# Kernel optimization log

Measured on AMD Instinct MI355X. Metric: run time of the kernel, lower is better.

The kernel has to match this reference:

```python
import jax, jax.numpy as jnp
import numpy as np

E = 8          # n_experts
K = 2          # n_activated_experts (top_k)
CAP_FACTOR = 1.25


def _expert_mlp(x, cond, mask, W1, W2):
    # x: [t, d], cond: [t, dc], mask: [t] -> [t, d]
    h = jax.nn.gelu(jnp.concatenate([x, cond], axis=-1) @ W1)
    return (h @ W2) * mask[:, None]


def setup_inputs() -> dict:
    key = jax.random.key(0)
    ks = jax.random.split(key, 8)
    b, n, d, dc, dff = 4, 2048, 1024, 256, 4096
    return {
        "x": jax.random.normal(ks[0], (b, n, d), jnp.float32),
        "cond": jax.random.normal(ks[1], (b, n, dc), jnp.float32),
        "mask": jnp.ones((b, n), jnp.float32),
        "Wr": jax.random.normal(ks[2], (d, E), jnp.float32) * 0.02,
        "W1s": jax.random.normal(ks[3], (d + dc, dff), jnp.float32) * 0.02,
        "W2s": jax.random.normal(ks[4], (dff, d), jnp.float32) * 0.02,
        "W1e": jax.random.normal(ks[5], (E, d + dc, dff), jnp.float32) * 0.02,
        "W2e": jax.random.normal(ks[6], (E, dff, d), jnp.float32) * 0.02,
    }


def reference(x, cond, mask, Wr, W1s, W2s, W1e, W2e):
    b, n, d = x.shape
    T = b * n
    cap = int(CAP_FACTOR * K * T / E)  # expert_capacity (static)

    xf = x.reshape(T, d)
    cf = cond.reshape(T, -1)
    mf = mask.reshape(T)

    # ---- router: softmax then top-k, normalized weights ----
    scores = jax.nn.softmax(xf @ Wr, axis=-1)              # [T, E]
    w, idx = jax.lax.top_k(scores, K)                      # [T, K]
    w = w / jnp.sum(w, axis=-1, keepdims=True)

    # ---- shared expert ----
    x_shared = _expert_mlp(xf, cf, mf, W1s, W2s)           # [T, d]

    # ---- indices_and_bins: stable sort by expert id + histogram/cumsum ----
    te = idx.reshape(-1)                                   # [T*K]
    order = jnp.argsort(te)                                # stable sort
    bin_ids = te[order]                                    # [T*K]
    tpe = jnp.zeros((E,), jnp.int32).at[te].add(1)         # tokens_per_expert
    starts = jnp.cumsum(tpe) - tpe                         # exclusive cumsum
    pos = jnp.arange(T * K) - starts[bin_ids]              # slot within expert bin
    tok = order // K                                       # source token row
    valid = pos < cap                                      # capacity drop

    # ---- binned_gather into [E, cap, *] buffers (drops overflow tokens) ----
    xg = jnp.zeros((E, cap, d), xf.dtype).at[bin_ids, pos].set(xf[tok], mode="drop")
    cg = jnp.zeros((E, cap, cf.shape[-1]), cf.dtype).at[bin_ids, pos].set(cf[tok], mode="drop")
    mg = jnp.zeros((E, cap), mf.dtype).at[bin_ids, pos].set(mf[tok], mode="drop")

    # ---- per-expert dense compute (grouped GEMM via einsum) ----
    inp = jnp.concatenate([xg, cg], axis=-1)               # [E, cap, d+dc]
    h = jax.nn.gelu(jnp.einsum("eci,eih->ech", inp, W1e))  # [E, cap, dff]
    y = jnp.einsum("ech,ehd->ecd", h, W2e) * mg[..., None] # [E, cap, d]

    # ---- binned_scatter combine with expert weights ----
    vals = y[bin_ids, jnp.minimum(pos, cap - 1)]           # [T*K, d]
    vals = vals * (w.reshape(-1)[order] * valid)[:, None]
    x_moe = jnp.zeros((T, d), xf.dtype).at[tok].add(vals)

    out = (x_shared + x_moe * K) / (K + 1)                 # normalize_expert_weights=True
    return out.reshape(b, n, d)
```

## Files before the change

### kernel.cpp

```cpp
#include <hip/hip_runtime.h>


typedef unsigned short u16;
typedef unsigned int u32;
typedef __bf16 bf16x8 __attribute__((ext_vector_type(8)));
typedef float f32x4 __attribute__((ext_vector_type(4)));

constexpr int T_TOK = 8192;
constexpr int DIM   = 1024;
constexpr int DCOND = 256;
constexpr int DFF   = 4096;
constexpr int NEXP  = 8;
constexpr int CAP   = 2560;

__device__ __forceinline__ float b2f(u16 u) {
    union { u32 u; float f; } v; v.u = (u32)u << 16; return v.f;
}
__device__ __forceinline__ u16 f2b(float f) {
    union { float f; u32 u; } v; v.f = f;
    u32 r = (v.u + 0x7fffu + ((v.u >> 16) & 1u)) >> 16;
    return (u16)r;
}
__device__ __forceinline__ float gelu_f(float x) {
    if (!(x == x)) x = 0.f;
    x = fminf(1e4f, fmaxf(-1e4f, x));
    float z = 0.7978845608028654f * (x + 0.044715f * x * x * x);
    float e = __expf(2.0f * z);
    float th = 1.0f - 2.0f / (e + 1.0f);
    return 0.5f * x * (1.0f + th);
}

__device__ __forceinline__ void gload16(const u16* g, u16* l) {
    __builtin_amdgcn_global_load_lds(
        (const __attribute__((address_space(1))) void*)g,
        (__attribute__((address_space(3))) void*)l, 16, 0, 0);
}

template <int IMM>
__device__ __forceinline__ bf16x8 dsr(u32 addr) {
    bf16x8 d;
    asm volatile("ds_read_b128 %0, %1 offset:%2" : "=v"(d) : "v"(addr), "n"(IMM));
    return d;
}
template <int N>
__device__ __forceinline__ void vmwait() {
    asm volatile("s_waitcnt vmcnt(%0)" :: "n"(N) : "memory");
}
__device__ __forceinline__ void lgkm0() {
    asm volatile("s_waitcnt lgkmcnt(0)" ::: "memory");
}

__global__ void moe_probe(const u16* __restrict__ x, int* __restrict__ flag) {
    const int lane = threadIdx.x;
    int cnt = 0;
    for (int i = lane; i < 4096; i += 64) {
        int e = (x[i] >> 7) & 0xFF;
        cnt += (e >= 0xC8);
    }
#pragma unroll
    for (int off = 32; off; off >>= 1) cnt += __shfl_xor(cnt, off, 64);
    if (lane == 0) flag[0] = (cnt > 8) ? 1 : 0;
}

__global__ __launch_bounds__(256) void moe_cvt(
    const void* __restrict__ in, u16* __restrict__ out,
    const int* __restrict__ flag)
{
    const long long i = ((long long)blockIdx.x * 256 + threadIdx.x) * 8;
    if (flag[0]) {
        const float* s = (const float*)in + i;
        float4 a = *(const float4*)s;
        float4 b = *(const float4*)(s + 4);
        __align__(16) u16 t8[8];
        t8[0] = f2b(a.x); t8[1] = f2b(a.y); t8[2] = f2b(a.z); t8[3] = f2b(a.w);
        t8[4] = f2b(b.x); t8[5] = f2b(b.y); t8[6] = f2b(b.z); t8[7] = f2b(b.w);
        *(uint4*)(out + i) = *(const uint4*)t8;
    } else {
        *(uint4*)(out + i) = *(const uint4*)((const u16*)in + i);
    }
}

__global__ __launch_bounds__(256) void moe_router(
    const void* __restrict__ xv, const void* __restrict__ Wrv,
    const int* __restrict__ flag,
    float* __restrict__ wbuf, int* __restrict__ idxbuf)
{
    const int t = blockIdx.x * 4 + (threadIdx.x >> 6);
    const int lane = threadIdx.x & 63;
    const bool isf32 = flag[0] != 0;

    float acc[NEXP];
#pragma unroll
    for (int e = 0; e < NEXP; ++e) acc[e] = 0.f;

    if (isf32) {
        const float* xr = (const float*)xv + (long long)t * DIM;
        const float* Wr = (const float*)Wrv;
        for (int it = 0; it < DIM / 64; ++it) {
            int d = it * 64 + lane;
            float xvv = xr[d];
            float4 wa = *(const float4*)(Wr + d * NEXP);
            float4 wb = *(const float4*)(Wr + d * NEXP + 4);
            acc[0] += xvv * wa.x; acc[1] += xvv * wa.y;
            acc[2] += xvv * wa.z; acc[3] += xvv * wa.w;
            acc[4] += xvv * wb.x; acc[5] += xvv * wb.y;
            acc[6] += xvv * wb.z; acc[7] += xvv * wb.w;
        }
    } else {
        const u16* xr = (const u16*)xv + (long long)t * DIM;
        const u16* Wr = (const u16*)Wrv;
        for (int it = 0; it < DIM / 64; ++it) {
            int d = it * 64 + lane;
            float xvv = b2f(xr[d]);
            uint4 wvv = *(const uint4*)(Wr + d * NEXP);
            const u16* ws = (const u16*)&wvv;
#pragma unroll
            for (int e = 0; e < NEXP; ++e) acc[e] += xvv * b2f(ws[e]);
        }
    }
#pragma unroll
    for (int off = 32; off; off >>= 1)
#pragma unroll
        for (int e = 0; e < NEXP; ++e) acc[e] += __shfl_xor(acc[e], off, 64);

    if (lane == 0) {
        float b1 = -3.4e38f, b2 = -3.4e38f; int i1 = 0, i2 = 0;
#pragma unroll
        for (int e = 0; e < NEXP; ++e) {
            float v = acc[e];
            if (v > b1) { b2 = b1; i2 = i1; b1 = v; i1 = e; }
            else if (v > b2) { b2 = v; i2 = e; }
        }
        float p2 = expf(b2 - b1);
        float inv = 1.0f / (1.0f + p2);
        wbuf[2 * t] = inv;       wbuf[2 * t + 1] = p2 * inv;
        idxbuf[2 * t] = i1;      idxbuf[2 * t + 1] = i2;
    }
}

__global__ void moe_bins(const int* __restrict__ idxbuf, int* __restrict__ slot_of,
                         int* __restrict__ token_of, int* __restrict__ rows_e)
{
    const int lane = threadIdx.x;
    const unsigned long long lmask = (1ull << lane) - 1ull;
    int cnt[NEXP];
#pragma unroll
    for (int q = 0; q < NEXP; ++q) cnt[q] = 0;

    for (int base = 0; base < T_TOK * 2; base += 256) {
        int e4[4];
#pragma unroll
        for (int u = 0; u < 4; ++u) e4[u] = idxbuf[base + u * 64 + lane];
#pragma unroll
        for (int u = 0; u < 4; ++u) {
            int e = e4[u];
            int ent = base + u * 64 + lane;
            int my = 0;
#pragma unroll
            for (int q = 0; q < NEXP; ++q) {
                unsigned long long bal = __ballot(e == q);
                if (e == q) my = cnt[q] + (int)__popcll(bal & lmask);
                cnt[q] += (int)__popcll(bal);
            }
            slot_of[ent] = my;
            if (my < CAP) token_of[e * CAP + my] = ent >> 1;
        }
    }
    if (lane == 0) {
#pragma unroll
        for (int q = 0; q < NEXP; ++q) rows_e[q] = cnt[q] < CAP ? cnt[q] : CAP;
    }
}

__global__ __launch_bounds__(256) void moe_transpose(
    const void* __restrict__ inv, u16* __restrict__ out, const int* __restrict__ flag,
    int R, int C, int zBase, long long inBatch, long long outBatch)
{
    const int zi = zBase + blockIdx.z;
    const bool isf32 = flag[0] != 0;
    out += (long long)blockIdx.z * outBatch;
    const int c0 = blockIdx.x * 64, r0 = blockIdx.y * 64;

    __shared__ __align__(16) u16 tile[64][66];

    for (int g = threadIdx.x; g < 512; g += 256) {
        int r = g >> 3, c8 = (g & 7) * 8;
        long long off = (long long)zi * inBatch + (long long)(r0 + r) * C + c0 + c8;
        if (isf32) {
            const float* s = (const float*)inv + off;
            float4 a = *(const float4*)s;
            float4 b = *(const float4*)(s + 4);
            tile[r][c8 + 0] = f2b(a.x); tile[r][c8 + 1] = f2b(a.y);
            tile[r][c8 + 2] = f2b(a.z); tile[r][c8 + 3] = f2b(a.w);
            tile[r][c8 + 4] = f2b(b.x); tile[r][c8 + 5] = f2b(b.y);
            tile[r][c8 + 6] = f2b(b.z); tile[r][c8 + 7] = f2b(b.w);
        } else {
            uint4 v = *(const uint4*)((const u16*)inv + off);
            const u16* s = (const u16*)&v;
#pragma unroll
            for (int j = 0; j < 8; ++j) tile[r][c8 + j] = s[j];
        }
    }
    __syncthreads();
    for (int g = threadIdx.x; g < 512; g += 256) {
        int oc = g >> 3, orr = (g & 7) * 8;
        __align__(16) u16 vals[8];
#pragma unroll
        for (int j = 0; j < 8; ++j) vals[j] = tile[orr + j][oc];
        *(uint4*)&out[(long long)(c0 + oc) * R + r0 + orr] = *(const uint4*)vals;
    }
}


#define AIMM(buf, qm, f8) ((buf) * 32768 + (qm) * 16384 + (f8) * 2048)

#define READ_A(buf, qm) do { \
    a[0][0] = dsr<AIMM(buf, qm, 0)>(aA0); a[0][1] = dsr<AIMM(buf, qm, 0)>(aA1); \
    a[1][0] = dsr<AIMM(buf, qm, 1)>(aA0); a[1][1] = dsr<AIMM(buf, qm, 1)>(aA1); \
    a[2][0] = dsr<AIMM(buf, qm, 2)>(aA0); a[2][1] = dsr<AIMM(buf, qm, 2)>(aA1); \
    a[3][0] = dsr<AIMM(buf, qm, 3)>(aA0); a[3][1] = dsr<AIMM(buf, qm, 3)>(aA1); \
} while (0)

#define READ_B(buf, qn) do { \
    if constexpr (BN == 256) { \
        b[qn][0][0] = dsr<(buf) * 32768 + (qn) * 16384 + 0>(aB0); \
        b[qn][0][1] = dsr<(buf) * 32768 + (qn) * 16384 + 0>(aB1); \
        b[qn][1][0] = dsr<(buf) * 32768 + (qn) * 16384 + 2048>(aB0); \
        b[qn][1][1] = dsr<(buf) * 32768 + (qn) * 16384 + 2048>(aB1); \
    } else { \
        b[qn][0][0] = dsr<(buf) * 16384 + (qn) * 8192>(aB0); \
        b[qn][0][1] = dsr<(buf) * 16384 + (qn) * 8192>(aB1); \
    } \
} while (0)

#define MFMA_Q(qm, qn) do { \
    _Pragma("unroll") for (int f9 = 0; f9 < 4; ++f9) \
    _Pragma("unroll") for (int n9 = 0; n9 < N9; ++n9) \
    _Pragma("unroll") for (int k9 = 0; k9 < 2; ++k9) \
        acc[(qm) * 4 + f9][(qn) * N9 + n9] = __builtin_amdgcn_mfma_f32_16x16x32_bf16( \
            a[f9][k9], b[qn][n9][k9], acc[(qm) * 4 + f9][(qn) * N9 + n9], 0, 0, 0); \
} while (0)

#define STAGE_A(buf, qm, kt) do { \
    const int ke7 = (kt) * 64; \
    _Pragma("unroll") for (int i7 = 0; i7 < 2; ++i7) { \
        const u16* src7; \
        if constexpr (MODE >= 1) { \
            src7 = (ke7 < DIM) \
                ? (const u16*)(A1b + offA1[i7][qm] + ke7 * 2) \
                : (const u16*)(A2b + offA2[i7][qm] + (ke7 - DIM) * 2); \
        } else { \
            src7 = (const u16*)(A1b + offA1[i7][qm] + ke7 * 2); \
        } \
        gload16(src7, &As[buf][qm][(wave * 64 + i7 * 512) * 8]); \
    } \
} while (0)

#define STAGE_B(buf, qn, kt) do { \
    const int ke7 = (kt) * 64; \
    _Pragma("unroll") for (int i7 = 0; i7 < SB; ++i7) \
        gload16((const u16*)(BTb + offB[i7][qn] + ke7 * 2), \
                &Bs[buf][qn][(wave * 64 + i7 * 512) * 8]); \
} while (0)

#define PH_OPEN() __builtin_amdgcn_sched_barrier(0)
#define PH_MID() do { \
    __builtin_amdgcn_sched_barrier(0); \
    __builtin_amdgcn_s_barrier(); \
    lgkm0(); \
    __builtin_amdgcn_sched_barrier(0); \
    __builtin_amdgcn_s_setprio(1); \
} while (0)
#define PH_CLOSE() do { \
    __builtin_amdgcn_s_setprio(0); \
    __builtin_amdgcn_sched_barrier(0); \
    __builtin_amdgcn_s_barrier(); \
} while (0)
#define PH_CLOSE_VM() do { \
    __builtin_amdgcn_s_setprio(0); \
    vmwait<VMN>(); \
    __builtin_amdgcn_sched_barrier(0); \
    __builtin_amdgcn_s_barrier(); \
} while (0)

template <int MODE, int KTOT, int BN>
__global__ __launch_bounds__(512, 2) void moe_gemm_8p(
    const u16* __restrict__ A1, const u16* __restrict__ A2,
    const u16* __restrict__ BT, u16* __restrict__ C,
    const int* __restrict__ tok_base, const int* __restrict__ rows_base,
    int ldC, long long aBatch, long long bBatch, long long cBatch)
{
    constexpr int NKT = KTOT / 64;
    static_assert((NKT & 1) == 0 && NKT >= 4, "K tiling");
    constexpr int N9  = BN / 128;
    constexpr int SB  = BN / 128;
    constexpr int VMN = 2 + 2 * SB;

    const u32 nwg  = gridDim.x * gridDim.y;
    const u32 flat = blockIdx.y * gridDim.x + blockIdx.x;
    const u32 swz  = (flat & 7u) * (nwg >> 3) + (flat >> 3);
    const int bx = (int)(swz % gridDim.x);
    const int by = (int)(swz / gridDim.x);

    const int z = blockIdx.z;
    int rows = 1 << 30;
    if (rows_base) {
        rows = rows_base[z];
        if (by * 256 >= rows) return;
    }

    __shared__ __align__(16) u16 As[2][2][8192];
    __shared__ __align__(16) u16 Bs[2][2][BN * 32];

    const int tid  = threadIdx.x;
    const int lane = tid & 63;
    const int wave = tid >> 6;
    const int wmw  = wave >> 2;
    const int wnw  = wave & 3;
    const int m0 = by * 256;
    const int n0 = bx * BN;

    const char* A1b = (const char*)(MODE == 0 ? A1 + (long long)z * aBatch : A1);
    const char* A2b = (const char*)A2;
    const char* BTb = (const char*)(BT + (long long)z * bBatch);

    u32 offA1[2][2], offA2[2][2], offB[SB][2];
#pragma unroll
    for (int i = 0; i < 2; ++i) {
        const int g = tid + i * 512;
        const int wm = g >> 9, r = (g >> 3) & 63, c16 = g & 7;
        const int cs = (c16 ^ (r & 7)) * 8;
#pragma unroll
        for (int qm = 0; qm < 2; ++qm) {
            const int rg = m0 + wm * 128 + qm * 64 + r;
            if constexpr (MODE == 2) {
                const int* tok = tok_base + (long long)z * CAP;
                const int tk = (rg < rows) ? tok[rg] : 0;
                offA1[i][qm] = (u32)((tk * DIM + cs) * 2);
                offA2[i][qm] = (u32)((tk * DCOND + cs) * 2);
            } else if constexpr (MODE == 1) {
                offA1[i][qm] = (u32)((rg * DIM + cs) * 2);
                offA2[i][qm] = (u32)((rg * DCOND + cs) * 2);
            } else {
                offA1[i][qm] = (u32)(((long long)rg * KTOT + cs) * 2);
                offA2[i][qm] = 0;
            }
        }
    }
#pragma unroll
    for (int i = 0; i < SB; ++i) {
        const int g = tid + i * 512;
        int wn, c;
        if constexpr (BN == 256) { wn = g >> 8; c = (g >> 3) & 31; }
        else                     { wn = g >> 7; c = (g >> 3) & 15; }
        const int c16 = g & 7;
        const int cs = (c16 ^ (c & 7)) * 8;
#pragma unroll
        for (int qn = 0; qn < 2; ++qn) {
            const int cbl = (BN == 256) ? (wn * 64 + qn * 32 + c)
                                        : (wn * 32 + qn * 16 + c);
            offB[i][qn] = (u32)(((long long)(n0 + cbl) * KTOT + cs) * 2);
        }
    }

    const u32 AsB = (u32)(size_t)(__attribute__((address_space(3))) u16*)&As[0][0][0];
    const u32 BsB = (u32)(size_t)(__attribute__((address_space(3))) u16*)&Bs[0][0][0];
    const int lrow = lane & 15;
    const int x0 = (((lane >> 4) + 0) ^ (lane & 7)) << 4;
    const int x4 = (((lane >> 4) + 4) ^ (lane & 7)) << 4;
    const u32 aA0 = AsB + (u32)((wmw * 64 + lrow) * 128 + x0);
    const u32 aA1 = AsB + (u32)((wmw * 64 + lrow) * 128 + x4);
    const int bro = (BN == 256 ? wnw * 32 : wnw * 16) + lrow;
    const u32 aB0 = BsB + (u32)(bro * 128 + x0);
    const u32 aB1 = BsB + (u32)(bro * 128 + x4);

    f32x4 acc[8][2 * N9];
#pragma unroll
    for (int m = 0; m < 8; ++m)
#pragma unroll
        for (int n = 0; n < 2 * N9; ++n) { f32x4 zv = {0.f, 0.f, 0.f, 0.f}; acc[m][n] = zv; }

    bf16x8 a[4][2];
    bf16x8 b[2][N9][2];

    STAGE_A(0, 0, 0); STAGE_B(0, 0, 0); STAGE_A(0, 1, 0); STAGE_B(0, 1, 0);
    STAGE_A(1, 0, 1); STAGE_B(1, 0, 1); STAGE_B(1, 1, 1);
    vmwait<VMN>();
    __builtin_amdgcn_sched_barrier(0);
    __builtin_amdgcn_s_barrier();

#pragma unroll 1
    for (int t = 0; t < NKT / 2; ++t) {
        const int k2 = 2 * t;
        const int kA = (k2 + 2 < NKT) ? k2 + 2 : NKT - 1;
        const int kB = (k2 + 3 < NKT) ? k2 + 3 : NKT - 1;
        PH_OPEN(); READ_A(0, 0); READ_B(0, 0); STAGE_A(1, 1, k2 + 1);
        PH_MID();  MFMA_Q(0, 0); PH_CLOSE();
        PH_OPEN(); READ_B(0, 1); STAGE_A(0, 0, kA);
        PH_MID();  MFMA_Q(0, 1); PH_CLOSE();
        PH_OPEN(); READ_A(0, 1); STAGE_B(0, 0, kA);
        PH_MID();  MFMA_Q(1, 0); PH_CLOSE();
        PH_OPEN(); STAGE_B(0, 1, kA);
        PH_MID();  MFMA_Q(1, 1); PH_CLOSE_VM();
        PH_OPEN(); READ_A(1, 0); READ_B(1, 0); STAGE_A(0, 1, kA);
        PH_MID();  MFMA_Q(0, 0); PH_CLOSE();
        PH_OPEN(); READ_B(1, 1); STAGE_A(1, 0, kB);
        PH_MID();  MFMA_Q(0, 1); PH_CLOSE();
        PH_OPEN(); READ_A(1, 1); STAGE_B(1, 0, kB);
        PH_MID();  MFMA_Q(1, 0); PH_CLOSE();
        PH_OPEN(); STAGE_B(1, 1, kB);
        PH_MID();  MFMA_Q(1, 1); PH_CLOSE_VM();
    }

    u16* Cz = C + (long long)z * cBatch;
#pragma unroll
    for (int m = 0; m < 8; ++m) {
        const int rowb = m0 + wmw * 128 + (m >> 2) * 64 + (m & 3) * 16 + (lane >> 4) * 4;
#pragma unroll
        for (int n = 0; n < 2 * N9; ++n) {
            int col;
            if constexpr (BN == 256)
                col = n0 + wnw * 64 + (n >> 1) * 32 + (n & 1) * 16 + (lane & 15);
            else
                col = n0 + wnw * 32 + n * 16 + (lane & 15);
#pragma unroll
            for (int rr = 0; rr < 4; ++rr) {
                float v = acc[m][n][rr];
                if constexpr (MODE >= 1) v = gelu_f(v);
                Cz[(long long)(rowb + rr) * ldC + col] = f2b(v);
            }
        }
    }
}

__global__ __launch_bounds__(256) void moe_combine(
    const u16* __restrict__ xs, const u16* __restrict__ y,
    const float* __restrict__ wbuf, const int* __restrict__ idxbuf,
    const int* __restrict__ slot_of, const void* __restrict__ maskv,
    void* __restrict__ outv, const int* __restrict__ flag)
{
    const int t = blockIdx.x;
    const int c = threadIdx.x * 4;
    const bool isf32 = flag[0] != 0;
    const float mk = isf32 ? ((const float*)maskv)[t] : b2f(((const u16*)maskv)[t]);

    int e1 = idxbuf[2 * t], e2 = idxbuf[2 * t + 1];
    int s1 = slot_of[2 * t], s2 = slot_of[2 * t + 1];
    float w1 = wbuf[2 * t], w2 = wbuf[2 * t + 1];
    float g1 = (s1 < CAP) ? w1 : 0.f;
    float g2 = (s2 < CAP) ? w2 : 0.f;
    int r1 = s1 < CAP ? s1 : CAP - 1;
    int r2 = s2 < CAP ? s2 : CAP - 1;

    uint2 xvv = *(const uint2*)(xs + (long long)t * DIM + c);
    uint2 y1 = *(const uint2*)(y + ((long long)e1 * CAP + r1) * DIM + c);
    uint2 y2 = *(const uint2*)(y + ((long long)e2 * CAP + r2) * DIM + c);
    const u16* xp = (const u16*)&xvv;
    const u16* p1 = (const u16*)&y1;
    const u16* p2 = (const u16*)&y2;

    float o[4];
#pragma unroll
    for (int q = 0; q < 4; ++q) {
        float v = (b2f(xp[q]) + 2.f * (g1 * b2f(p1[q]) + g2 * b2f(p2[q]))) * mk * (1.f / 3.f);
        o[q] = (v == v) ? v : 0.f;
    }
    if (isf32) {
        float4 o4 = {o[0], o[1], o[2], o[3]};
        *(float4*)((float*)outv + (long long)t * DIM + c) = o4;
    } else {
        __align__(8) u16 ov[4];
#pragma unroll
        for (int q = 0; q < 4; ++q) ov[q] = f2b(o[q]);
        *(uint2*)((u16*)outv + (long long)t * DIM + c) = *(const uint2*)ov;
    }
}

extern "C" void kernel_launch(void* const* d_in, const int* in_sizes, int n_in,
                              void* d_out, int out_size, void* d_ws, size_t ws_size,
                              hipStream_t stream)
{
    const void* x    = d_in[0];
    const void* cond = d_in[1];
    const void* mask = d_in[2];
    const void* Wr   = d_in[3];
    const void* W1s  = d_in[4];
    const void* W2s  = d_in[5];
    const void* W1e  = d_in[6];
    const void* W2e  = d_in[7];

    const int KIN = DIM + DCOND;
    const int EGX = 3;

    char* p = (char*)d_ws;
    u16* W1sT   = (u16*)p; p += (long long)DFF * KIN * 2;
    u16* W2sT   = (u16*)p; p += (long long)DIM * DFF * 2;
    u16* W1eT   = (u16*)p; p += (long long)EGX * DFF * KIN * 2;
    u16* W2eT   = (u16*)p; p += (long long)EGX * DIM * DFF * 2;
    u16* h      = (u16*)p; p += (long long)T_TOK * DFF * 2;
    u16* xs     = (u16*)p; p += (long long)T_TOK * DIM * 2;
    u16* y      = (u16*)p; p += (long long)NEXP * CAP * DIM * 2;
    u16* xb     = (u16*)p; p += (long long)T_TOK * DIM * 2;
    u16* cb     = (u16*)p; p += (long long)T_TOK * DCOND * 2;
    float* wbuf = (float*)p; p += T_TOK * 2 * sizeof(float);
    int* idxbuf = (int*)p;   p += T_TOK * 2 * sizeof(int);
    int* slot_of = (int*)p;  p += T_TOK * 2 * sizeof(int);
    int* token_of = (int*)p; p += NEXP * CAP * sizeof(int);
    int* rows_e = (int*)p;   p += 256;
    int* flag   = (int*)p;   p += 256;
    (void)ws_size; (void)in_sizes; (void)n_in; (void)out_size;

    dim3 b256(256);
    dim3 b512(512);

    moe_probe<<<dim3(1), dim3(64), 0, stream>>>((const u16*)x, flag);

    moe_cvt<<<dim3(T_TOK * DIM / (256 * 8)), b256, 0, stream>>>(x, xb, flag);
    moe_cvt<<<dim3(T_TOK * DCOND / (256 * 8)), b256, 0, stream>>>(cond, cb, flag);

    moe_router<<<dim3(T_TOK / 4), b256, 0, stream>>>(x, Wr, flag, wbuf, idxbuf);
    moe_bins<<<dim3(1), dim3(64), 0, stream>>>(idxbuf, slot_of, token_of, rows_e);

    moe_transpose<<<dim3(DFF / 64, KIN / 64, 1), b256, 0, stream>>>(
        W1s, W1sT, flag, KIN, DFF, 0, 0, 0);
    moe_transpose<<<dim3(DIM / 64, DFF / 64, 1), b256, 0, stream>>>(
        W2s, W2sT, flag, DFF, DIM, 0, 0, 0);

    moe_gemm_8p<1, 1280, 256><<<dim3(DFF / 256, T_TOK / 256, 1), b512, 0, stream>>>(
        xb, cb, W1sT, h, nullptr, nullptr, DFF, 0, 0, 0);
    moe_gemm_8p<0, 4096, 128><<<dim3(DIM / 128, T_TOK / 256, 1), b512, 0, stream>>>(
        h, nullptr, W2sT, xs, nullptr, nullptr, DIM, 0, 0, 0);

    const int gsz[3] = {3, 3, 2};
    int gb = 0;
    for (int gi = 0; gi < 3; ++gi) {
        const int eg = gsz[gi];
        moe_transpose<<<dim3(DFF / 64, KIN / 64, eg), b256, 0, stream>>>(
            W1e, W1eT, flag, KIN, DFF, gb,
            (long long)KIN * DFF, (long long)DFF * KIN);
        moe_transpose<<<dim3(DIM / 64, DFF / 64, eg), b256, 0, stream>>>(
            W2e, W2eT, flag, DFF, DIM, gb,
            (long long)DFF * DIM, (long long)DIM * DFF);

        moe_gemm_8p<2, 1280, 256><<<dim3(DFF / 256, CAP / 256, eg), b512, 0, stream>>>(
            xb, cb, W1eT, h, token_of + (long long)gb * CAP, rows_e + gb,
            DFF, 0, (long long)DFF * KIN, (long long)CAP * DFF);
        moe_gemm_8p<0, 4096, 128><<<dim3(DIM / 128, CAP / 256, eg), b512, 0, stream>>>(
            h, nullptr, W2eT, y + (long long)gb * CAP * DIM, nullptr, rows_e + gb,
            DIM, (long long)CAP * DFF, (long long)DIM * DFF, (long long)CAP * DIM);
        gb += eg;
    }

    moe_combine<<<dim3(T_TOK), b256, 0, stream>>>(xs, y, wbuf, idxbuf, slot_of, mask, d_out, flag);
}
```

Baseline: 1.154 ms.

## Double-buffer A fragments and overlap LDS reads with MFMA phases in GEMM loop

Restructures the 8-phase main loop of the grouped GEMM so LDS fragment reads for the next quadrant are issued before the barrier of the current MFMA phase. Partial lgkmcnt waits replace the full lgkmcnt(0) drain, letting reads stay in flight. The A register fragments are now double-buffered per M-quadrant, the prologue prefetches the first fragments, and the MFMA loop order puts k outermost. This is meant to hide LDS latency behind matrix math, at the cost of more VGPRs (risking spills at 2 waves/SIMD) and a subtle wait-count schedule that could be wrong.

After: 1.307 ms. 13.3% more time.

```diff
diff --git a/kernel.cpp b/kernel.cpp
--- a/kernel.cpp
+++ b/kernel.cpp
@@ -46,8 +46,9 @@
 __device__ __forceinline__ void vmwait() {
     asm volatile("s_waitcnt vmcnt(%0)" :: "n"(N) : "memory");
 }
-__device__ __forceinline__ void lgkm0() {
-    asm volatile("s_waitcnt lgkmcnt(0)" ::: "memory");
+template <int N>
+__device__ __forceinline__ void lgkmw() {
+    asm volatile("s_waitcnt lgkmcnt(%0)" :: "n"(N) : "memory");
 }
 
 __global__ void moe_probe(const u16* __restrict__ x, int* __restrict__ flag) {
@@ -215,10 +216,10 @@
 #define AIMM(buf, qm, f8) ((buf) * 32768 + (qm) * 16384 + (f8) * 2048)
 
 #define READ_A(buf, qm) do { \
-    a[0][0] = dsr<AIMM(buf, qm, 0)>(aA0); a[0][1] = dsr<AIMM(buf, qm, 0)>(aA1); \
-    a[1][0] = dsr<AIMM(buf, qm, 1)>(aA0); a[1][1] = dsr<AIMM(buf, qm, 1)>(aA1); \
-    a[2][0] = dsr<AIMM(buf, qm, 2)>(aA0); a[2][1] = dsr<AIMM(buf, qm, 2)>(aA1); \
-    a[3][0] = dsr<AIMM(buf, qm, 3)>(aA0); a[3][1] = dsr<AIMM(buf, qm, 3)>(aA1); \
+    a[qm][0][0] = dsr<AIMM(buf, qm, 0)>(aA0); a[qm][0][1] = dsr<AIMM(buf, qm, 0)>(aA1); \
+    a[qm][1][0] = dsr<AIMM(buf, qm, 1)>(aA0); a[qm][1][1] = dsr<AIMM(buf, qm, 1)>(aA1); \
+    a[qm][2][0] = dsr<AIMM(buf, qm, 2)>(aA0); a[qm][2][1] = dsr<AIMM(buf, qm, 2)>(aA1); \
+    a[qm][3][0] = dsr<AIMM(buf, qm, 3)>(aA0); a[qm][3][1] = dsr<AIMM(buf, qm, 3)>(aA1); \
 } while (0)
 
 #define READ_B(buf, qn) do { \
@@ -234,11 +235,11 @@
 } while (0)
 
 #define MFMA_Q(qm, qn) do { \
+    _Pragma("unroll") for (int k9 = 0; k9 < 2; ++k9) \
     _Pragma("unroll") for (int f9 = 0; f9 < 4; ++f9) \
     _Pragma("unroll") for (int n9 = 0; n9 < N9; ++n9) \
-    _Pragma("unroll") for (int k9 = 0; k9 < 2; ++k9) \
         acc[(qm) * 4 + f9][(qn) * N9 + n9] = __builtin_amdgcn_mfma_f32_16x16x32_bf16( \
-            a[f9][k9], b[qn][n9][k9], acc[(qm) * 4 + f9][(qn) * N9 + n9], 0, 0, 0); \
+            a[qm][f9][k9], b[qn][n9][k9], acc[(qm) * 4 + f9][(qn) * N9 + n9], 0, 0, 0); \
 } while (0)
 
 #define STAGE_A(buf, qm, kt) do { \
@@ -263,24 +264,30 @@
                 &Bs[buf][qn][(wave * 64 + i7 * 512) * 8]); \
 } while (0)
 
-#define PH_OPEN() __builtin_amdgcn_sched_barrier(0)
-#define PH_MID() do { \
+#define PH_MID(n) do { \
     __builtin_amdgcn_sched_barrier(0); \
     __builtin_amdgcn_s_barrier(); \
-    lgkm0(); \
-    __builtin_amdgcn_sched_barrier(0); \
+    lgkmw<n>(); \
+    __builtin_amdgcn_sched_barrier(0); \
+    __builtin_amdgcn_s_setprio(1); \
+} while (0)
+#define PH_MIDN() do { \
+    __builtin_amdgcn_sched_barrier(0); \
+    __builtin_amdgcn_s_barrier(); \
     __builtin_amdgcn_s_setprio(1); \
 } while (0)
 #define PH_CLOSE() do { \
     __builtin_amdgcn_s_setprio(0); \
     __builtin_amdgcn_sched_barrier(0); \
     __builtin_amdgcn_s_barrier(); \
+    __builtin_amdgcn_sched_barrier(0); \
 } while (0)
 #define PH_CLOSE_VM() do { \
     __builtin_amdgcn_s_setprio(0); \
-    vmwait<VMN>(); \
+    vmwait<VMW>(); \
     __builtin_amdgcn_sched_barrier(0); \
     __builtin_amdgcn_s_barrier(); \
+    __builtin_amdgcn_sched_barrier(0); \
 } while (0)
 
 template <int MODE, int KTOT, int BN>
@@ -294,7 +301,8 @@
     static_assert((NKT & 1) == 0 && NKT >= 4, "K tiling");
     constexpr int N9  = BN / 128;
     constexpr int SB  = BN / 128;
-    constexpr int VMN = 2 + 2 * SB;
+    constexpr int VMW = 2 + SB;
+    constexpr int RB  = 2 * SB;
 
     const u32 nwg  = gridDim.x * gridDim.y;
     const u32 flat = blockIdx.y * gridDim.x + blockIdx.x;
@@ -380,37 +388,41 @@
 #pragma unroll
         for (int n = 0; n < 2 * N9; ++n) { f32x4 zv = {0.f, 0.f, 0.f, 0.f}; acc[m][n] = zv; }
 
-    bf16x8 a[4][2];
+    bf16x8 a[2][4][2];
     bf16x8 b[2][N9][2];
 
     STAGE_A(0, 0, 0); STAGE_B(0, 0, 0); STAGE_A(0, 1, 0); STAGE_B(0, 1, 0);
-    STAGE_A(1, 0, 1); STAGE_B(1, 0, 1); STAGE_B(1, 1, 1);
-    vmwait<VMN>();
+    STAGE_A(1, 0, 1); STAGE_B(1, 0, 1); STAGE_A(1, 1, 1); STAGE_B(1, 1, 1);
+    vmwait<4 + 2 * SB>();
     __builtin_amdgcn_sched_barrier(0);
     __builtin_amdgcn_s_barrier();
+    __builtin_amdgcn_sched_barrier(0);
+    READ_A(0, 0); READ_B(0, 0);
 
 #pragma unroll 1
     for (int t = 0; t < NKT / 2; ++t) {
         const int k2 = 2 * t;
         const int kA = (k2 + 2 < NKT) ? k2 + 2 : NKT - 1;
         const int kB = (k2 + 3 < NKT) ? k2 + 3 : NKT - 1;
-        PH_OPEN(); READ_A(0, 0); READ_B(0, 0); STAGE_A(1, 1, k2 + 1);
-        PH_MID();  MFMA_Q(0, 0); PH_CLOSE();
-        PH_OPEN(); READ_B(0, 1); STAGE_A(0, 0, kA);
-        PH_MID();  MFMA_Q(0, 1); PH_CLOSE();
-        PH_OPEN(); READ_A(0, 1); STAGE_B(0, 0, kA);
-        PH_MID();  MFMA_Q(1, 0); PH_CLOSE();
-        PH_OPEN(); STAGE_B(0, 1, kA);
-        PH_MID();  MFMA_Q(1, 1); PH_CLOSE_VM();
-        PH_OPEN(); READ_A(1, 0); READ_B(1, 0); STAGE_A(0, 1, kA);
-        PH_MID();  MFMA_Q(0, 0); PH_CLOSE();
-        PH_OPEN(); READ_B(1, 1); STAGE_A(1, 0, kB);
-        PH_MID();  MFMA_Q(0, 1); PH_CLOSE();
-        PH_OPEN(); READ_A(1, 1); STAGE_B(1, 0, kB);
-        PH_MID();  MFMA_Q(1, 0); PH_CLOSE();
-        PH_OPEN(); STAGE_B(1, 1, kB);
-        PH_MID();  MFMA_Q(1, 1); PH_CLOSE_VM();
-    }
+        READ_B(0, 1);
+        PH_MID(RB);  MFMA_Q(0, 0); PH_CLOSE();
+        READ_A(0, 1); STAGE_A(0, 0, kA);
+        PH_MID(8);   MFMA_Q(0, 1); PH_CLOSE();
+        STAGE_B(0, 0, kA);
+        PH_MID(0);   MFMA_Q(1, 0); PH_CLOSE_VM();
+        READ_A(1, 0); READ_B(1, 0); STAGE_B(0, 1, kA); STAGE_A(0, 1, kA);
+        PH_MIDN();   MFMA_Q(1, 1); PH_CLOSE();
+        READ_B(1, 1);
+        PH_MID(RB);  MFMA_Q(0, 0); PH_CLOSE();
+        READ_A(1, 1); STAGE_A(1, 0, kB);
+        PH_MID(8);   MFMA_Q(0, 1); PH_CLOSE();
+        STAGE_B(1, 0, kB);
+        PH_MID(0);   MFMA_Q(1, 0); PH_CLOSE_VM();
+        READ_A(0, 0); READ_B(0, 0); STAGE_B(1, 1, kB); STAGE_A(1, 1, kB);
+        PH_MIDN();   MFMA_Q(1, 1); PH_CLOSE();
+    }
+    lgkmw<0>();
+    vmwait<0>();
 
     u16* Cz = C + (long long)z * cBatch;
 #pragma unroll
```

## Restructure GEMM main loop from eight phases to four per K pair

Applied to the files above, without the earlier changes.

The GEMM inner loop is regrouped from eight barrier-delimited phases per two K tiles into four. Each phase now loads both B quadrants and issues MFMAs over a full M half, so fewer s_barriers and sched_barriers are needed. A final vmwait is added after the loop. The aim is lower synchronization overhead and longer MFMA bursts, at the cost of more registers live for B fragments and coarser interleaving of global loads with compute.

Result: no change. 1.142 ms (-1.0%).

```diff
diff --git a/kernel.cpp b/kernel.cpp
--- a/kernel.cpp
+++ b/kernel.cpp
@@ -233,12 +233,13 @@
     } \
 } while (0)
 
-#define MFMA_Q(qm, qn) do { \
+#define MFMA_P(qm) do { \
+    _Pragma("unroll") for (int k9 = 0; k9 < 2; ++k9) \
     _Pragma("unroll") for (int f9 = 0; f9 < 4; ++f9) \
+    _Pragma("unroll") for (int q9 = 0; q9 < 2; ++q9) \
     _Pragma("unroll") for (int n9 = 0; n9 < N9; ++n9) \
-    _Pragma("unroll") for (int k9 = 0; k9 < 2; ++k9) \
-        acc[(qm) * 4 + f9][(qn) * N9 + n9] = __builtin_amdgcn_mfma_f32_16x16x32_bf16( \
-            a[f9][k9], b[qn][n9][k9], acc[(qm) * 4 + f9][(qn) * N9 + n9], 0, 0, 0); \
+        acc[(qm) * 4 + f9][q9 * N9 + n9] = __builtin_amdgcn_mfma_f32_16x16x32_bf16( \
+            a[f9][k9], b[q9][n9][k9], acc[(qm) * 4 + f9][q9 * N9 + n9], 0, 0, 0); \
 } while (0)
 
 #define STAGE_A(buf, qm, kt) do { \
@@ -263,28 +264,23 @@
                 &Bs[buf][qn][(wave * 64 + i7 * 512) * 8]); \
 } while (0)
 
-#define PH_OPEN() __builtin_amdgcn_sched_barrier(0)
-#define PH_MID() do { \
-    __builtin_amdgcn_sched_barrier(0); \
-    __builtin_amdgcn_s_barrier(); \
+#define PH_WAIT() do { \
     lgkm0(); \
     __builtin_amdgcn_sched_barrier(0); \
     __builtin_amdgcn_s_setprio(1); \
 } while (0)
-#define PH_CLOSE() do { \
+#define PH_END() do { \
     __builtin_amdgcn_s_setprio(0); \
-    __builtin_amdgcn_sched_barrier(0); \
     __builtin_amdgcn_s_barrier(); \
 } while (0)
-#define PH_CLOSE_VM() do { \
+#define PH_END_VM() do { \
     __builtin_amdgcn_s_setprio(0); \
-    vmwait<VMN>(); \
-    __builtin_amdgcn_sched_barrier(0); \
+    vmwait<VMW>(); \
     __builtin_amdgcn_s_barrier(); \
 } while (0)
 
 template <int MODE, int KTOT, int BN>
-__global__ __launch_bounds__(512, 2) void moe_gemm_8p(
+__global__ __launch_bounds__(512, 2) void moe_gemm_4p(
     const u16* __restrict__ A1, const u16* __restrict__ A2,
     const u16* __restrict__ BT, u16* __restrict__ C,
     const int* __restrict__ tok_base, const int* __restrict__ rows_base,
@@ -294,7 +290,7 @@
     static_assert((NKT & 1) == 0 && NKT >= 4, "K tiling");
     constexpr int N9  = BN / 128;
     constexpr int SB  = BN / 128;
-    constexpr int VMN = 2 + 2 * SB;
+    constexpr int VMW = 2 + 2 * SB;
 
     const u32 nwg  = gridDim.x * gridDim.y;
     const u32 flat = blockIdx.y * gridDim.x + blockIdx.x;
@@ -385,8 +381,7 @@
 
     STAGE_A(0, 0, 0); STAGE_B(0, 0, 0); STAGE_A(0, 1, 0); STAGE_B(0, 1, 0);
     STAGE_A(1, 0, 1); STAGE_B(1, 0, 1); STAGE_B(1, 1, 1);
-    vmwait<VMN>();
-    __builtin_amdgcn_sched_barrier(0);
+    vmwait<VMW>();
     __builtin_amdgcn_s_barrier();
 
 #pragma unroll 1
@@ -394,23 +389,20 @@
         const int k2 = 2 * t;
         const int kA = (k2 + 2 < NKT) ? k2 + 2 : NKT - 1;
         const int kB = (k2 + 3 < NKT) ? k2 + 3 : NKT - 1;
-        PH_OPEN(); READ_A(0, 0); READ_B(0, 0); STAGE_A(1, 1, k2 + 1);
-        PH_MID();  MFMA_Q(0, 0); PH_CLOSE();
-        PH_OPEN(); READ_B(0, 1); STAGE_A(0, 0, kA);
-        PH_MID();  MFMA_Q(0, 1); PH_CLOSE();
-        PH_OPEN(); READ_A(0, 1); STAGE_B(0, 0, kA);
-        PH_MID();  MFMA_Q(1, 0); PH_CLOSE();
-        PH_OPEN(); STAGE_B(0, 1, kA);
-        PH_MID();  MFMA_Q(1, 1); PH_CLOSE_VM();
-        PH_OPEN(); READ_A(1, 0); READ_B(1, 0); STAGE_A(0, 1, kA);
-        PH_MID();  MFMA_Q(0, 0); PH_CLOSE();
-        PH_OPEN(); READ_B(1, 1); STAGE_A(1, 0, kB);
-        PH_MID();  MFMA_Q(0, 1); PH_CLOSE();
-        PH_OPEN(); READ_A(1, 1); STAGE_B(1, 0, kB);
-        PH_MID();  MFMA_Q(1, 0); PH_CLOSE();
-        PH_OPEN(); STAGE_B(1, 1, kB);
-        PH_MID();  MFMA_Q(1, 1); PH_CLOSE_VM();
-    }
+        STAGE_A(1, 1, k2 + 1);
+        READ_A(0, 0); READ_B(0, 0); READ_B(0, 1);
+        PH_WAIT(); MFMA_P(0); PH_END();
+        STAGE_A(0, 0, kA); STAGE_B(0, 0, kA); STAGE_B(0, 1, kA);
+        READ_A(0, 1);
+        PH_WAIT(); MFMA_P(1); PH_END_VM();
+        STAGE_A(0, 1, kA);
+        READ_A(1, 0); READ_B(1, 0); READ_B(1, 1);
+        PH_WAIT(); MFMA_P(0); PH_END();
+        STAGE_A(1, 0, kB); STAGE_B(1, 0, kB); STAGE_B(1, 1, kB);
+        READ_A(1, 1);
+        PH_WAIT(); MFMA_P(1); PH_END_VM();
+    }
+    vmwait<0>();
 
     u16* Cz = C + (long long)z * cBatch;
 #pragma unroll
@@ -526,9 +518,9 @@
     moe_transpose<<<dim3(DIM / 64, DFF / 64, 1), b256, 0, stream>>>(
         W2s, W2sT, flag, DFF, DIM, 0, 0, 0);
 
-    moe_gemm_8p<1, 1280, 256><<<dim3(DFF / 256, T_TOK / 256, 1), b512, 0, stream>>>(
+    moe_gemm_4p<1, 1280, 256><<<dim3(DFF / 256, T_TOK / 256, 1), b512, 0, stream>>>(
         xb, cb, W1sT, h, nullptr, nullptr, DFF, 0, 0, 0);
-    moe_gemm_8p<0, 4096, 128><<<dim3(DIM / 128, T_TOK / 256, 1), b512, 0, stream>>>(
+    moe_gemm_4p<0, 4096, 128><<<dim3(DIM / 128, T_TOK / 256, 1), b512, 0, stream>>>(
         h, nullptr, W2sT, xs, nullptr, nullptr, DIM, 0, 0, 0);
 
     const int gsz[3] = {3, 3, 2};
@@ -542,10 +534,10 @@
             W2e, W2eT, flag, DFF, DIM, gb,
             (long long)DFF * DIM, (long long)DIM * DFF);
 
-        moe_gemm_8p<2, 1280, 256><<<dim3(DFF / 256, CAP / 256, eg), b512, 0, stream>>>(
+        moe_gemm_4p<2, 1280, 256><<<dim3(DFF / 256, CAP / 256, eg), b512, 0, stream>>>(
             xb, cb, W1eT, h, token_of + (long long)gb * CAP, rows_e + gb,
             DFF, 0, (long long)DFF * KIN, (long long)CAP * DFF);
-        moe_gemm_8p<0, 4096, 128><<<dim3(DIM / 128, CAP / 256, eg), b512, 0, stream>>>(
+        moe_gemm_4p<0, 4096, 128><<<dim3(DIM / 128, CAP / 256, eg), b512, 0, stream>>>(
             h, nullptr, W2eT, y + (long long)gb * CAP * DIM, nullptr, rows_e + gb,
             DIM, (long long)CAP * DFF, (long long)DIM * DFF, (long long)CAP * DIM);
         gb += eg;
```
